# Performance work log

Measured on AMD Instinct MI355X. Metric: run time of the kernel, lower is better.

## Reference

```python
import jax, jax.numpy as jnp
import numpy as np
import math

B, S, D, H = 2, 2048, 1024, 16
DH = D // H
NEG = -1e9


def gelu(x):
    return 0.5 * x * (1.0 + jnp.tanh(math.sqrt(2.0 / math.pi) * (x + 0.044715 * x ** 3)))


def layernorm(x, g, b, eps=1e-6):
    # faithful to module: uses std (unbiased, N-1) and adds eps to std, not var
    mean = jnp.mean(x, axis=-1, keepdims=True)
    var = jnp.sum((x - mean) ** 2, axis=-1, keepdims=True) / (x.shape[-1] - 1)
    std = jnp.sqrt(var)
    return g * (x - mean) / (std + eps) + b


def setup_inputs() -> dict:
    key = jax.random.key(0)
    ks = jax.random.split(key, 13)
    sd = 0.02
    return {
        "x": jax.random.normal(ks[0], (B, S, D), jnp.float32),
        "w_attn": jax.random.normal(ks[1], (D, 3 * D), jnp.float32) * sd,
        "b_attn": jnp.zeros((3 * D,), jnp.float32),
        "w_aproj": jax.random.normal(ks[2], (D, D), jnp.float32) * sd,
        "b_aproj": jnp.zeros((D,), jnp.float32),
        "g1": jnp.ones((D,), jnp.float32),
        "b1": jnp.zeros((D,), jnp.float32),
        "w_fc": jax.random.normal(ks[3], (D, 4 * D), jnp.float32) * sd,
        "b_fc": jnp.zeros((4 * D,), jnp.float32),
        "w_mproj": jax.random.normal(ks[4], (4 * D, D), jnp.float32) * sd,
        "b_mproj": jnp.zeros((D,), jnp.float32),
        "g2": jnp.ones((D,), jnp.float32),
        "b2": jnp.zeros((D,), jnp.float32),
    }


def reference(x, w_attn, b_attn, w_aproj, b_aproj, g1, b1, w_fc, b_fc, w_mproj, b_mproj, g2, b2):
    # --- attention ---
    qkv = x @ w_attn + b_attn                       # [B,S,3D]
    q, k, v = jnp.split(qkv, 3, axis=2)
    q = q.reshape(B, S, H, DH).transpose(0, 2, 1, 3)  # [B,H,S,DH]
    k = k.reshape(B, S, H, DH).transpose(0, 2, 1, 3)
    v = v.reshape(B, S, H, DH).transpose(0, 2, 1, 3)
    w = jnp.einsum('bhqd,bhkd->bhqk', q, k) / math.sqrt(DH)
    mask = jnp.tril(jnp.ones((S, S), jnp.float32))[None, None]
    w = w * mask + NEG * (1.0 - mask)
    w = jax.nn.softmax(w, axis=-1)
    a = jnp.einsum('bhqk,bhkd->bhqd', w, v)         # [B,H,S,DH]
    a = a.transpose(0, 2, 1, 3).reshape(B, S, D)
    a = a @ w_aproj + b_aproj
    # --- postLN + MLP ---
    n = layernorm(x + a, g1, b1)
    h = gelu(n @ w_fc + b_fc)
    m = h @ w_mproj + b_mproj
    return layernorm(n + m, g2, b2)
```

## Files before the change

### kernel.cpp

```cpp
#include <hip/hip_runtime.h>
#include <type_traits>


typedef unsigned short u16;
typedef short s16x8 __attribute__((ext_vector_type(8)));
typedef unsigned short u16x4 __attribute__((ext_vector_type(4)));
typedef float f32x4 __attribute__((ext_vector_type(4)));
typedef float f32x16 __attribute__((ext_vector_type(16)));

__device__ __forceinline__ u16 f2b(float f) {
    union { float f; unsigned u; } x{f};
    unsigned r = x.u + 0x7FFFu + ((x.u >> 16) & 1u);
    return (u16)(r >> 16);
}

__device__ __forceinline__ f32x4 mfma16(s16x8 a, s16x8 b, f32x4 c) {
    return __builtin_amdgcn_mfma_f32_16x16x32_bf16(a, b, c, 0, 0, 0);
}

__device__ __forceinline__ f32x16 mfma32(s16x8 a, s16x8 b, f32x16 c) {
    return __builtin_amdgcn_mfma_f32_32x32x16_bf16(a, b, c, 0, 0, 0);
}

__device__ __forceinline__ int cvtpk(float a, float b) {
    int r;
    asm("v_cvt_pk_bf16_f32 %0, %1, %2" : "=v"(r) : "v"(a), "v"(b));
    return r;
}

__device__ __forceinline__ void gld_lds16(const u16* g, u16* l) {
    __builtin_amdgcn_global_load_lds(
        (const __attribute__((address_space(1))) void*)g,
        (__attribute__((address_space(3))) void*)l, 16, 0, 0);
}

__global__ __launch_bounds__(256) void cvt_bf16(const float* __restrict__ in,
                                                u16* __restrict__ out, int n4) {
    int i = blockIdx.x * 256 + threadIdx.x;
    if (i < n4) {
        float4 v = ((const float4*)in)[i];
        u16x4 o = {f2b(v.x), f2b(v.y), f2b(v.z), f2b(v.w)};
        ((u16x4*)out)[i] = o;
    }
}

__global__ __launch_bounds__(256) void transpose_bf16(const float* __restrict__ W,
                                                      u16* __restrict__ WT,
                                                      int K, int N) {
    __shared__ float t[32][33];
    int tx = threadIdx.x & 31, ty = threadIdx.x >> 5;
    int n0 = blockIdx.x * 32, k0 = blockIdx.y * 32;
    #pragma unroll
    for (int r = ty; r < 32; r += 8)
        t[r][tx] = W[(size_t)(k0 + r) * N + n0 + tx];
    __syncthreads();
    #pragma unroll
    for (int r = ty; r < 32; r += 8)
        WT[(size_t)(n0 + r) * K + k0 + tx] = f2b(t[tx][r]);
}

template<int BN, bool GELU, typename OT>
__global__ __launch_bounds__(256) void gemm_db(const u16* __restrict__ A,
                                               const u16* __restrict__ BT,
                                               const float* __restrict__ bias,
                                               OT* __restrict__ C,
                                               int M, int N, int K, int ldc) {
    constexpr int NF = BN / 32;
    constexpr int BNI = BN / 32;
    __shared__ u16 As[2][128 * 64];
    __shared__ u16 Bs[2][BN * 64];

    int t = threadIdx.x;
    int w = t >> 6, l = t & 63, l16 = l & 15, lh = l >> 4;
    int wr = w >> 1, wc = w & 1;

    int nbm = M >> 7;
    int cpx = gridDim.x >> 3;
    int id = blockIdx.x;
    int id2 = (id & 7) * cpx + (id >> 3);
    size_t m0 = (size_t)(id2 % nbm) * 128;
    size_t n0 = (size_t)(id2 / nbm) * BN;

    int rowA = t >> 3;
    int gc = t & 7;
    int gc2 = gc ^ (((rowA >> 2) & 1) << 1) ^ (((rowA >> 3) & 1) << 2);
    const u16* Ag = A + (m0 + rowA) * (size_t)K + gc2 * 8;
    const u16* Bg = BT + (n0 + rowA) * (size_t)K + gc2 * 8;
    int wbase = w * 512;

    f32x4 acc[4][NF] = {};
    int cxor = (((l16 >> 2) & 1) << 4) ^ (((l16 >> 3) & 1) << 5);

    #pragma unroll
    for (int j = 0; j < 4; ++j)
        gld_lds16(Ag + (size_t)j * 32 * K, &As[0][j * 2048 + wbase]);
    #pragma unroll
    for (int j = 0; j < BNI; ++j)
        gld_lds16(Bg + (size_t)j * 32 * K, &Bs[0][j * 2048 + wbase]);
    __syncthreads();

    int cur = 0;
    for (int k0 = 0; k0 < K; k0 += 64) {
        if (k0 + 64 < K) {
            const u16* Ap = Ag + k0 + 64;
            #pragma unroll
            for (int j = 0; j < 4; ++j)
                gld_lds16(Ap + (size_t)j * 32 * K, &As[cur ^ 1][j * 2048 + wbase]);
            const u16* Bp = Bg + k0 + 64;
            #pragma unroll
            for (int j = 0; j < BNI; ++j)
                gld_lds16(Bp + (size_t)j * 32 * K, &Bs[cur ^ 1][j * 2048 + wbase]);
        }
        __builtin_amdgcn_s_setprio(1);
        #pragma unroll
        for (int ks = 0; ks < 2; ++ks) {
            s16x8 af[4], bf[NF];
            #pragma unroll
            for (int fm = 0; fm < 4; ++fm) {
                int row = wr * 64 + fm * 16 + l16;
                int col = (ks * 32 + lh * 8) ^ cxor;
                af[fm] = *(const s16x8*)&As[cur][row * 64 + col];
            }
            #pragma unroll
            for (int fn = 0; fn < NF; ++fn) {
                int row = wc * (BN / 2) + fn * 16 + l16;
                int col = (ks * 32 + lh * 8) ^ cxor;
                bf[fn] = *(const s16x8*)&Bs[cur][row * 64 + col];
            }
            #pragma unroll
            for (int fm = 0; fm < 4; ++fm)
                #pragma unroll
                for (int fn = 0; fn < NF; ++fn)
                    acc[fm][fn] = mfma16(af[fm], bf[fn], acc[fm][fn]);
        }
        __builtin_amdgcn_s_setprio(0);
        __syncthreads();
        cur ^= 1;
    }

    #pragma unroll
    for (int fn = 0; fn < NF; ++fn) {
        size_t col = n0 + wc * (BN / 2) + fn * 16 + l16;
        float bs = bias[col];
        #pragma unroll
        for (int fm = 0; fm < 4; ++fm) {
            size_t row0 = m0 + wr * 64 + fm * 16 + lh * 4;
            #pragma unroll
            for (int i = 0; i < 4; ++i) {
                float v = acc[fm][fn][i] + bs;
                if constexpr (GELU) {
                    float x3 = v * v * v;
                    v = 0.5f * v * (1.f + tanhf(0.7978845608f * (v + 0.044715f * x3)));
                }
                if constexpr (std::is_same<OT, u16>::value)
                    C[(row0 + i) * ldc + col] = f2b(v);
                else
                    C[(row0 + i) * ldc + col] = v;
            }
        }
    }
}

__global__ __launch_bounds__(256) void attn_kernel(const u16* __restrict__ qkv,
                                                   u16* __restrict__ abuf) {
    constexpr int S = 2048, D3 = 3072, Dm = 1024;
    __shared__ u16 Kl[64 * 64];
    __shared__ u16 Vt[64 * 64];

    int t = threadIdx.x;
    int w = t >> 6, l = t & 63;
    int l32 = l & 31, hi = l >> 5;
    int qt = 15 - (int)(blockIdx.x >> 5);
    int bh = blockIdx.x & 31;
    int b = bh >> 4, h = bh & 15;
    int qb = qt * 128 + w * 32;
    size_t base = (size_t)b * S * D3;

    s16x8 qf[4];
    const u16* qp = qkv + base + (size_t)(qb + l32) * D3 + h * 64 + hi * 8;
    #pragma unroll
    for (int kk = 0; kk < 4; ++kk)
        qf[kk] = *(const s16x8*)(qp + kk * 16);

    f32x16 O0 = {}, O1 = {};
    float m = -1e30f, lr = 0.f;
    constexpr float cexp = 0.18033688011112042f;
    constexpr float THR = 64.0f;

    int rK = t >> 2, gK = t & 3;
    int sK0 = gK ^ (rK & 7), sK1 = (gK + 4) ^ (rK & 7);
    const u16* kgp = qkv + base + (size_t)rK * D3 + Dm + h * 64;
    int cv = w * 16;

    int nst = 2 * (qt + 1);
    for (int sc = 0; sc < nst; ++sc) {
        int kvb = sc * 64;
        if (sc) __syncthreads();
        {
            const u16* kp = kgp + (size_t)kvb * D3;
            s16x8 a0 = *(const s16x8*)(kp + sK0 * 8);
            s16x8 a1 = *(const s16x8*)(kp + sK1 * 8);
            *(s16x8*)&Kl[rK * 64 + gK * 8] = a0;
            *(s16x8*)&Kl[rK * 64 + (gK + 4) * 8] = a1;
        }
        {
            const u16* vp = qkv + base + (size_t)(kvb + l) * D3 + 2 * Dm + h * 64 + cv;
            s16x8 v0 = *(const s16x8*)vp;
            s16x8 v1 = *(const s16x8*)(vp + 8);
            #pragma unroll
            for (int e = 0; e < 8; ++e) {
                int d0 = cv + e, d1 = cv + 8 + e;
                Vt[d0 * 64 + (l ^ ((d0 & 7) << 3))] = (u16)v0[e];
                Vt[d1 * 64 + (l ^ ((d1 & 7) << 3))] = (u16)v1[e];
            }
        }
        __syncthreads();

        #pragma unroll
        for (int ti = 0; ti < 2; ++ti) {
            int kvt = kvb + ti * 32;
            if (kvt > qb) continue;
            bool diag = (kvt == qb);

            f32x16 sa = {};
            #pragma unroll
            for (int kk = 0; kk < 4; ++kk) {
                int r = ti * 32 + l32;
                s16x8 kf = *(const s16x8*)&Kl[r * 64 + (((2 * kk + hi) ^ (r & 7)) * 8)];
                sa = mfma32(kf, qf[kk], sa);
            }

            float p[16];
            float mx = -1e30f;
            #pragma unroll
            for (int reg = 0; reg < 16; ++reg) {
                int kvloc = (reg & 3) + 8 * (reg >> 2) + 4 * hi;
                float s = sa[reg];
                if (diag && kvloc > l32) s = -1e30f;
                p[reg] = s;
                mx = fmaxf(mx, s);
            }
            mx = fmaxf(mx, __shfl_xor(mx, 32));

            bool skip = __all(mx <= m + THR);
            if (!skip) {
                float mn = fmaxf(m, mx);
                float a_ = exp2f(cexp * (m - mn));
                m = mn;
                #pragma unroll
                for (int reg = 0; reg < 16; ++reg) {
                    int src = (reg & 3) + 8 * (reg >> 2) + 4 * hi;
                    float aq = __shfl(a_, src);
                    O0[reg] *= aq;
                    O1[reg] *= aq;
                }
                lr *= a_;
            }
            float rs = 0.f;
            #pragma unroll
            for (int reg = 0; reg < 16; ++reg) {
                p[reg] = exp2f(cexp * (p[reg] - m));
                rs += p[reg];
            }
            rs += __shfl_xor(rs, 32);
            lr += rs;

            s16x8 pa[2];
            #pragma unroll
            for (int kk = 0; kk < 2; ++kk) {
                int pk01 = cvtpk(p[kk * 8 + 0], p[kk * 8 + 1]);
                int pk23 = cvtpk(p[kk * 8 + 2], p[kk * 8 + 3]);
                int pk45 = cvtpk(p[kk * 8 + 4], p[kk * 8 + 5]);
                int pk67 = cvtpk(p[kk * 8 + 6], p[kk * 8 + 7]);
                int sx01 = __shfl_xor(pk01, 32);
                int sx23 = __shfl_xor(pk23, 32);
                int sx45 = __shfl_xor(pk45, 32);
                int sx67 = __shfl_xor(pk67, 32);
                union { int i[4]; s16x8 v; } u;
                u.i[0] = hi ? sx45 : pk01;
                u.i[1] = hi ? sx67 : pk23;
                u.i[2] = hi ? pk45 : sx01;
                u.i[3] = hi ? pk67 : sx23;
                pa[kk] = u.v;
            }

            #pragma unroll
            for (int kk = 0; kk < 2; ++kk) {
                int d0 = l32;
                s16x8 vb0 = *(const s16x8*)&Vt[d0 * 64 + (((ti * 4 + kk * 2 + hi) ^ (d0 & 7)) * 8)];
                O0 = mfma32(pa[kk], vb0, O0);
                int d1 = 32 + l32;
                s16x8 vb1 = *(const s16x8*)&Vt[d1 * 64 + (((ti * 4 + kk * 2 + hi) ^ (d1 & 7)) * 8)];
                O1 = mfma32(pa[kk], vb1, O1);
            }
        }
    }

    float invl = 1.f / lr;
    size_t obase = (size_t)b * S * 1024 + h * 64;
    #pragma unroll
    for (int reg = 0; reg < 16; ++reg) {
        int src = (reg & 3) + 8 * (reg >> 2) + 4 * hi;
        float iq = __shfl(invl, src);
        size_t row = obase + (size_t)(qb + src) * 1024;
        abuf[row + l32] = f2b(O0[reg] * iq);
        abuf[row + 32 + l32] = f2b(O1[reg] * iq);
    }
}

template<bool WB>
__global__ __launch_bounds__(256) void resln(const float* __restrict__ xa,
                                             const float* __restrict__ xb2,
                                             const float* __restrict__ g,
                                             const float* __restrict__ be,
                                             float* __restrict__ outf,
                                             u16* __restrict__ outb) {
    int row = blockIdx.x;
    int t = threadIdx.x;
    size_t base = (size_t)row * 1024 + t * 4;
    float4 va = *(const float4*)(xa + base);
    float4 vb = *(const float4*)(xb2 + base);
    float v0 = va.x + vb.x, v1 = va.y + vb.y, v2 = va.z + vb.z, v3 = va.w + vb.w;
    float s1 = v0 + v1 + v2 + v3;
    float s2 = v0 * v0 + v1 * v1 + v2 * v2 + v3 * v3;
    #pragma unroll
    for (int off = 32; off >= 1; off >>= 1) {
        s1 += __shfl_down(s1, off);
        s2 += __shfl_down(s2, off);
    }
    __shared__ float r1[4], r2[4];
    if ((t & 63) == 0) { r1[t >> 6] = s1; r2[t >> 6] = s2; }
    __syncthreads();
    s1 = r1[0] + r1[1] + r1[2] + r1[3];
    s2 = r2[0] + r2[1] + r2[2] + r2[3];
    float mean = s1 * (1.f / 1024.f);
    float var = fmaxf((s2 - 1024.f * mean * mean) * (1.f / 1023.f), 0.f);
    float inv = 1.f / (sqrtf(var) + 1e-6f);
    int col = t * 4;
    float y0 = g[col + 0] * ((v0 - mean) * inv) + be[col + 0];
    float y1 = g[col + 1] * ((v1 - mean) * inv) + be[col + 1];
    float y2 = g[col + 2] * ((v2 - mean) * inv) + be[col + 2];
    float y3 = g[col + 3] * ((v3 - mean) * inv) + be[col + 3];
    float4 o = {y0, y1, y2, y3};
    *(float4*)(outf + base) = o;
    if constexpr (WB) {
        u16x4 ob = {f2b(y0), f2b(y1), f2b(y2), f2b(y3)};
        *(u16x4*)(outb + base) = ob;
    }
}

extern "C" void kernel_launch(void* const* d_in, const int* in_sizes, int n_in,
                              void* d_out, int out_size, void* d_ws, size_t ws_size,
                              hipStream_t stream) {
    (void)in_sizes; (void)n_in; (void)out_size; (void)ws_size;
    const float* x       = (const float*)d_in[0];
    const float* w_attn  = (const float*)d_in[1];
    const float* b_attn  = (const float*)d_in[2];
    const float* w_aproj = (const float*)d_in[3];
    const float* b_aproj = (const float*)d_in[4];
    const float* g1      = (const float*)d_in[5];
    const float* b1      = (const float*)d_in[6];
    const float* w_fc    = (const float*)d_in[7];
    const float* b_fc    = (const float*)d_in[8];
    const float* w_mproj = (const float*)d_in[9];
    const float* b_mproj = (const float*)d_in[10];
    const float* g2      = (const float*)d_in[11];
    const float* b2      = (const float*)d_in[12];
    float* out = (float*)d_out;

    constexpr int M = 4096;
    constexpr int D = 1024;

    char* ws = (char*)d_ws;
    u16*   slotA = (u16*)ws;
    char*  pB    = ws + (32u << 20);
    char*  pC    = ws + (40u << 20);
    char*  pD    = ws + (48u << 20);
    char*  pE    = ws + (64u << 20);

    u16*   xb   = (u16*)pB;
    u16*   wT   = (u16*)pC;
    u16*   qkv  = slotA;
    u16*   abuf = (u16*)pB;
    float* aout = (float*)pD;
    float* nbuf = (float*)pE;
    u16*   nb   = (u16*)pB;
    u16*   h    = slotA;
    float* mout = (float*)pD;

    dim3 blk(256);

    cvt_bf16<<<dim3(4096), blk, 0, stream>>>(x, xb, M * D / 4);

    transpose_bf16<<<dim3(3072 / 32, 1024 / 32), blk, 0, stream>>>(w_attn, wT, 1024, 3072);
    gemm_db<128, false, u16><<<dim3((M / 128) * (3072 / 128)), blk, 0, stream>>>(
        xb, wT, b_attn, qkv, M, 3072, 1024, 3072);

    attn_kernel<<<dim3(512), blk, 0, stream>>>(qkv, abuf);

    transpose_bf16<<<dim3(1024 / 32, 1024 / 32), blk, 0, stream>>>(w_aproj, wT, 1024, 1024);
    gemm_db<64, false, float><<<dim3((M / 128) * (1024 / 64)), blk, 0, stream>>>(
        abuf, wT, b_aproj, aout, M, 1024, 1024, 1024);

    resln<true><<<dim3(M), blk, 0, stream>>>(x, aout, g1, b1, nbuf, nb);

    transpose_bf16<<<dim3(4096 / 32, 1024 / 32), blk, 0, stream>>>(w_fc, wT, 1024, 4096);
    gemm_db<128, true, u16><<<dim3((M / 128) * (4096 / 128)), blk, 0, stream>>>(
        nb, wT, b_fc, h, M, 4096, 1024, 4096);

    transpose_bf16<<<dim3(1024 / 32, 4096 / 32), blk, 0, stream>>>(w_mproj, wT, 4096, 1024);
    gemm_db<64, false, float><<<dim3((M / 128) * (1024 / 64)), blk, 0, stream>>>(
        h, wT, b_mproj, mout, M, 1024, 4096, 1024);

    resln<false><<<dim3(M), blk, 0, stream>>>(nbuf, mout, g2, b2, out, nullptr);
}
```

Baseline: 314.2 us.

## Pair causal query tiles per block and double-buffer K/V with async LDS loads

The attention kernel now launches 256 blocks, and each block handles two query tiles (pr and 15-pr), so every block does about the same amount of causal work. K/V tiles are double-buffered in shared memory. K is loaded directly to LDS with gld_lds16 and V is prefetched into registers while the current tile is being computed, which overlaps global-load latency with MFMA work. Both 32-row sub-tiles of a 64-row chunk are scored together, which cuts syncs and loop overhead. The trade-offs are twice the LDS, higher register pressure, and only 256 blocks, one per CU with launch bounds (256,1), which may leave occupancy low.

```diff
diff --git a/kernel.cpp b/kernel.cpp
--- a/kernel.cpp
+++ b/kernel.cpp
@@ -161,150 +161,193 @@
     }
 }
 
-__global__ __launch_bounds__(256) void attn_kernel(const u16* __restrict__ qkv,
-                                                   u16* __restrict__ abuf) {
+__global__ __launch_bounds__(256, 1) void attn_kernel(const u16* __restrict__ qkv,
+                                                      u16* __restrict__ abuf) {
     constexpr int S = 2048, D3 = 3072, Dm = 1024;
-    __shared__ u16 Kl[64 * 64];
-    __shared__ u16 Vt[64 * 64];
+    __shared__ u16 Kl[2][64 * 64];
+    __shared__ u16 Vt[2][64 * 64];
 
     int t = threadIdx.x;
     int w = t >> 6, l = t & 63;
     int l32 = l & 31, hi = l >> 5;
-    int qt = 15 - (int)(blockIdx.x >> 5);
+    int pr = blockIdx.x >> 5;
     int bh = blockIdx.x & 31;
     int b = bh >> 4, h = bh & 15;
-    int qb = qt * 128 + w * 32;
     size_t base = (size_t)b * S * D3;
 
-    s16x8 qf[4];
-    const u16* qp = qkv + base + (size_t)(qb + l32) * D3 + h * 64 + hi * 8;
-    #pragma unroll
-    for (int kk = 0; kk < 4; ++kk)
-        qf[kk] = *(const s16x8*)(qp + kk * 16);
-
-    f32x16 O0 = {}, O1 = {};
-    float m = -1e30f, lr = 0.f;
+    int rK0 = t >> 3, gK = t & 7;
+    int rK1 = rK0 + 32;
+    size_t koff0 = (size_t)rK0 * D3 + (size_t)((gK ^ (rK0 & 7)) * 8);
+    size_t koff1 = (size_t)rK1 * D3 + (size_t)((gK ^ (rK1 & 7)) * 8);
+    const u16* kbase = qkv + base + Dm + h * 64;
+    const u16* vbase = qkv + base + 2 * Dm + h * 64 + w * 16;
+
     constexpr float cexp = 0.18033688011112042f;
     constexpr float THR = 64.0f;
-
-    int rK = t >> 2, gK = t & 3;
-    int sK0 = gK ^ (rK & 7), sK1 = (gK + 4) ^ (rK & 7);
-    const u16* kgp = qkv + base + (size_t)rK * D3 + Dm + h * 64;
-    int cv = w * 16;
-
-    int nst = 2 * (qt + 1);
-    for (int sc = 0; sc < nst; ++sc) {
-        int kvb = sc * 64;
-        if (sc) __syncthreads();
+    int xg = l32 & 7;
+
+    #pragma unroll 1
+    for (int ph = 0; ph < 2; ++ph) {
+        int qt = ph ? (15 - pr) : pr;
+        int qb = qt * 128 + w * 32;
+        int nst = 2 * (qt + 1);
+
+        s16x8 qf[4];
+        const u16* qp = qkv + base + (size_t)(qb + l32) * D3 + h * 64 + hi * 8;
+        #pragma unroll
+        for (int kk = 0; kk < 4; ++kk)
+            qf[kk] = *(const s16x8*)(qp + kk * 16);
+
+        f32x16 O0 = {}, O1 = {};
+        float m = -1e30f, lr = 0.f;
+
+        gld_lds16(kbase + koff0, &Kl[0][w * 512]);
+        gld_lds16(kbase + koff1, &Kl[0][2048 + w * 512]);
         {
-            const u16* kp = kgp + (size_t)kvb * D3;
-            s16x8 a0 = *(const s16x8*)(kp + sK0 * 8);
-            s16x8 a1 = *(const s16x8*)(kp + sK1 * 8);
-            *(s16x8*)&Kl[rK * 64 + gK * 8] = a0;
-            *(s16x8*)&Kl[rK * 64 + (gK + 4) * 8] = a1;
-        }
-        {
-            const u16* vp = qkv + base + (size_t)(kvb + l) * D3 + 2 * Dm + h * 64 + cv;
-            s16x8 v0 = *(const s16x8*)vp;
-            s16x8 v1 = *(const s16x8*)(vp + 8);
+            const u16* vp = vbase + (size_t)l * D3;
+            s16x8 pv0 = *(const s16x8*)vp;
+            s16x8 pv1 = *(const s16x8*)(vp + 8);
             #pragma unroll
             for (int e = 0; e < 8; ++e) {
-                int d0 = cv + e, d1 = cv + 8 + e;
-                Vt[d0 * 64 + (l ^ ((d0 & 7) << 3))] = (u16)v0[e];
-                Vt[d1 * 64 + (l ^ ((d1 & 7) << 3))] = (u16)v1[e];
+                int d0 = w * 16 + e, d1 = w * 16 + 8 + e;
+                Vt[0][d0 * 64 + (l ^ ((d0 & 7) << 3))] = (u16)pv0[e];
+                Vt[0][d1 * 64 + (l ^ ((d1 & 7) << 3))] = (u16)pv1[e];
             }
         }
         __syncthreads();
 
+        #pragma unroll 1
+        for (int sc = 0; sc < nst; ++sc) {
+            int cur = sc & 1;
+            bool pre = (sc + 1 < nst);
+            s16x8 v0, v1;
+            if (pre) {
+                size_t koffc = (size_t)(sc + 1) * 64 * D3;
+                gld_lds16(kbase + koffc + koff0, &Kl[cur ^ 1][w * 512]);
+                gld_lds16(kbase + koffc + koff1, &Kl[cur ^ 1][2048 + w * 512]);
+                const u16* vp = vbase + (size_t)((sc + 1) * 64 + l) * D3;
+                v0 = *(const s16x8*)vp;
+                v1 = *(const s16x8*)(vp + 8);
+            }
+
+            int kvb = sc * 64;
+            int navail = ((qb - kvb) >> 5) + 1;
+            if (navail > 0) {
+                if (navail > 2) navail = 2;
+                const u16* Kc = Kl[cur];
+                const u16* Vc = Vt[cur];
+                f32x16 sa0 = {}, sa1 = {};
+                #pragma unroll
+                for (int kk = 0; kk < 4; ++kk) {
+                    s16x8 kf = *(const s16x8*)&Kc[l32 * 64 + (((2 * kk + hi) ^ xg) * 8)];
+                    sa0 = mfma32(kf, qf[kk], sa0);
+                }
+                if (navail == 2) {
+                    #pragma unroll
+                    for (int kk = 0; kk < 4; ++kk) {
+                        s16x8 kf = *(const s16x8*)&Kc[(32 + l32) * 64 + (((2 * kk + hi) ^ xg) * 8)];
+                        sa1 = mfma32(kf, qf[kk], sa1);
+                    }
+                }
+                bool diag0 = (kvb == qb);
+                bool diag1 = (kvb + 32 == qb);
+                float p[32];
+                float mx = -1e30f;
+                #pragma unroll
+                for (int reg = 0; reg < 16; ++reg) {
+                    int kvloc = (reg & 3) + 8 * (reg >> 2) + 4 * hi;
+                    float s0 = sa0[reg];
+                    if (diag0 && kvloc > l32) s0 = -1e30f;
+                    p[reg] = s0;
+                    mx = fmaxf(mx, s0);
+                }
+                if (navail == 2) {
+                    #pragma unroll
+                    for (int reg = 0; reg < 16; ++reg) {
+                        int kvloc = (reg & 3) + 8 * (reg >> 2) + 4 * hi;
+                        float s1 = sa1[reg];
+                        if (diag1 && kvloc > l32) s1 = -1e30f;
+                        p[16 + reg] = s1;
+                        mx = fmaxf(mx, s1);
+                    }
+                }
+                mx = fmaxf(mx, __shfl_xor(mx, 32));
+                if (!__all(mx <= m + THR)) {
+                    float mn = fmaxf(m, mx);
+                    float a_ = exp2f(cexp * (m - mn));
+                    m = mn;
+                    #pragma unroll
+                    for (int reg = 0; reg < 16; ++reg) {
+                        int src = (reg & 3) + 8 * (reg >> 2) + 4 * hi;
+                        float aq = __shfl(a_, src);
+                        O0[reg] *= aq;
+                        O1[reg] *= aq;
+                    }
+                    lr *= a_;
+                }
+                float rs = 0.f;
+                #pragma unroll
+                for (int reg = 0; reg < 16; ++reg) {
+                    p[reg] = exp2f(cexp * (p[reg] - m));
+                    rs += p[reg];
+                }
+                if (navail == 2) {
+                    #pragma unroll
+                    for (int reg = 16; reg < 32; ++reg) {
+                        p[reg] = exp2f(cexp * (p[reg] - m));
+                        rs += p[reg];
+                    }
+                }
+                rs += __shfl_xor(rs, 32);
+                lr += rs;
+
+                #pragma unroll
+                for (int c = 0; c < 4; ++c) {
+                    if (c < navail * 2) {
+                        int pb = (c >> 1) * 16 + (c & 1) * 8;
+                        int pk01 = cvtpk(p[pb + 0], p[pb + 1]);
+                        int pk23 = cvtpk(p[pb + 2], p[pb + 3]);
+                        int pk45 = cvtpk(p[pb + 4], p[pb + 5]);
+                        int pk67 = cvtpk(p[pb + 6], p[pb + 7]);
+                        int sx01 = __shfl_xor(pk01, 32);
+                        int sx23 = __shfl_xor(pk23, 32);
+                        int sx45 = __shfl_xor(pk45, 32);
+                        int sx67 = __shfl_xor(pk67, 32);
+                        union { int i[4]; s16x8 v; } u;
+                        u.i[0] = hi ? sx45 : pk01;
+                        u.i[1] = hi ? sx67 : pk23;
+                        u.i[2] = hi ? pk45 : sx01;
+                        u.i[3] = hi ? pk67 : sx23;
+                        int go = ((c * 2 + hi) ^ xg) * 8;
+                        s16x8 vb0 = *(const s16x8*)&Vc[l32 * 64 + go];
+                        O0 = mfma32(u.v, vb0, O0);
+                        s16x8 vb1 = *(const s16x8*)&Vc[(32 + l32) * 64 + go];
+                        O1 = mfma32(u.v, vb1, O1);
+                    }
+                }
+            }
+
+            if (pre) {
+                #pragma unroll
+                for (int e = 0; e < 8; ++e) {
+                    int d0 = w * 16 + e, d1 = w * 16 + 8 + e;
+                    Vt[cur ^ 1][d0 * 64 + (l ^ ((d0 & 7) << 3))] = (u16)v0[e];
+                    Vt[cur ^ 1][d1 * 64 + (l ^ ((d1 & 7) << 3))] = (u16)v1[e];
+                }
+            }
+            __syncthreads();
+        }
+
+        float invl = 1.f / lr;
+        size_t obase = (size_t)b * S * 1024 + h * 64;
         #pragma unroll
-        for (int ti = 0; ti < 2; ++ti) {
-            int kvt = kvb + ti * 32;
-            if (kvt > qb) continue;
-            bool diag = (kvt == qb);
-
-            f32x16 sa = {};
-            #pragma unroll
-            for (int kk = 0; kk < 4; ++kk) {
-                int r = ti * 32 + l32;
-                s16x8 kf = *(const s16x8*)&Kl[r * 64 + (((2 * kk + hi) ^ (r & 7)) * 8)];
-                sa = mfma32(kf, qf[kk], sa);
-            }
-
-            float p[16];
-            float mx = -1e30f;
-            #pragma unroll
-            for (int reg = 0; reg < 16; ++reg) {
-                int kvloc = (reg & 3) + 8 * (reg >> 2) + 4 * hi;
-                float s = sa[reg];
-                if (diag && kvloc > l32) s = -1e30f;
-                p[reg] = s;
-                mx = fmaxf(mx, s);
-            }
-            mx = fmaxf(mx, __shfl_xor(mx, 32));
-
-            bool skip = __all(mx <= m + THR);
-            if (!skip) {
-                float mn = fmaxf(m, mx);
-                float a_ = exp2f(cexp * (m - mn));
-                m = mn;
-                #pragma unroll
-                for (int reg = 0; reg < 16; ++reg) {
-                    int src = (reg & 3) + 8 * (reg >> 2) + 4 * hi;
-                    float aq = __shfl(a_, src);
-                    O0[reg] *= aq;
-                    O1[reg] *= aq;
-                }
-                lr *= a_;
-            }
-            float rs = 0.f;
-            #pragma unroll
-            for (int reg = 0; reg < 16; ++reg) {
-                p[reg] = exp2f(cexp * (p[reg] - m));
-                rs += p[reg];
-            }
-            rs += __shfl_xor(rs, 32);
-            lr += rs;
-
-            s16x8 pa[2];
-            #pragma unroll
-            for (int kk = 0; kk < 2; ++kk) {
-                int pk01 = cvtpk(p[kk * 8 + 0], p[kk * 8 + 1]);
-                int pk23 = cvtpk(p[kk * 8 + 2], p[kk * 8 + 3]);
-                int pk45 = cvtpk(p[kk * 8 + 4], p[kk * 8 + 5]);
-                int pk67 = cvtpk(p[kk * 8 + 6], p[kk * 8 + 7]);
-                int sx01 = __shfl_xor(pk01, 32);
-                int sx23 = __shfl_xor(pk23, 32);
-                int sx45 = __shfl_xor(pk45, 32);
-                int sx67 = __shfl_xor(pk67, 32);
-                union { int i[4]; s16x8 v; } u;
-                u.i[0] = hi ? sx45 : pk01;
-                u.i[1] = hi ? sx67 : pk23;
-                u.i[2] = hi ? pk45 : sx01;
-                u.i[3] = hi ? pk67 : sx23;
-                pa[kk] = u.v;
-            }
-
-            #pragma unroll
-            for (int kk = 0; kk < 2; ++kk) {
-                int d0 = l32;
-                s16x8 vb0 = *(const s16x8*)&Vt[d0 * 64 + (((ti * 4 + kk * 2 + hi) ^ (d0 & 7)) * 8)];
-                O0 = mfma32(pa[kk], vb0, O0);
-                int d1 = 32 + l32;
-                s16x8 vb1 = *(const s16x8*)&Vt[d1 * 64 + (((ti * 4 + kk * 2 + hi) ^ (d1 & 7)) * 8)];
-                O1 = mfma32(pa[kk], vb1, O1);
-            }
-        }
-    }
-
-    float invl = 1.f / lr;
-    size_t obase = (size_t)b * S * 1024 + h * 64;
-    #pragma unroll
-    for (int reg = 0; reg < 16; ++reg) {
-        int src = (reg & 3) + 8 * (reg >> 2) + 4 * hi;
-        float iq = __shfl(invl, src);
-        size_t row = obase + (size_t)(qb + src) * 1024;
-        abuf[row + l32] = f2b(O0[reg] * iq);
-        abuf[row + 32 + l32] = f2b(O1[reg] * iq);
+        for (int reg = 0; reg < 16; ++reg) {
+            int src = (reg & 3) + 8 * (reg >> 2) + 4 * hi;
+            float iq = __shfl(invl, src);
+            size_t row = obase + (size_t)(qb + src) * 1024;
+            abuf[row + l32] = f2b(O0[reg] * iq);
+            abuf[row + 32 + l32] = f2b(O1[reg] * iq);
+        }
     }
 }
 
@@ -396,7 +439,7 @@
     gemm_db<128, false, u16><<<dim3((M / 128) * (3072 / 128)), blk, 0, stream>>>(
         xb, wT, b_attn, qkv, M, 3072, 1024, 3072);
 
-    attn_kernel<<<dim3(512), blk, 0, stream>>>(qkv, abuf);
+    attn_kernel<<<dim3(256), blk, 0, stream>>>(qkv, abuf);
 
     transpose_bf16<<<dim3(1024 / 32, 1024 / 32), blk, 0, stream>>>(w_aproj, wT, 1024, 1024);
     gemm_db<64, false, float><<<dim3((M / 128) * (1024 / 64)), blk, 0, stream>>>(
```

Result: no change. 314.1 us (-0.0%).
